# Performance work log

Hardware: AMD Instinct MI355X
Metric: run time of the kernel (lower is better)

The kernel has to match this reference:

```python
import jax, jax.numpy as jnp
import numpy as np

B, NV, DM, DK, DV, H, DFF = 256, 40, 512, 256, 256, 4, 2048
K1, K2 = 4, 8
EPS = 1e-5


def _knn_mask(vertices, k):
    # square_distance(xyz, xyz): dist[b,i,j] = ||x_i - x_j||^2
    d = -2.0 * jnp.einsum('bic,bjc->bij', vertices, vertices)
    sq = jnp.sum(vertices ** 2, -1)
    d = d + sq[:, :, None] + sq[:, None, :]
    # torch.topk(dist, k, dim=1, largest=False)[1].transpose(1,2) -> [B,N,k]
    idx = jax.lax.top_k(-jnp.swapaxes(d, 1, 2), k)[1]
    counts = jax.nn.one_hot(idx, NV, dtype=jnp.float32).sum(-2)  # [B,N,NV]
    return (counts < 1.0)[:, None, :, :]  # [B,1,N,N], broadcasts over heads (== repeat)


def _ln(x, g, b):
    m = x.mean(-1, keepdims=True)
    v = x.var(-1, keepdims=True)
    return (x - m) / jnp.sqrt(v + EPS) * g + b


def _encoder(x, mask, wq, bq, wk, bk, wv, bv, wo, bo, ln1g, ln1b, w1, b1, w2, b2, ln2g, ln2b):
    Bn, N, _ = x.shape
    q = (x @ wq + bq).reshape(Bn, N, H, DK).transpose(0, 2, 1, 3)   # [B,H,N,DK]
    kk = (x @ wk + bk).reshape(Bn, N, H, DK).transpose(0, 2, 3, 1)  # [B,H,DK,N]
    v = (x @ wv + bv).reshape(Bn, N, H, DV).transpose(0, 2, 1, 3)   # [B,H,N,DV]
    att = jnp.matmul(q, kk) / np.sqrt(DK)                           # [B,H,N,N]
    att = jnp.where(mask, -jnp.inf, att)
    att = jax.nn.softmax(att, axis=-1)
    o = jnp.matmul(att, v).transpose(0, 2, 1, 3).reshape(Bn, N, H * DV) @ wo + bo
    x = _ln(x + o, ln1g, ln1b)                                      # residual + LayerNorm
    ff = jax.nn.relu(x @ w1 + b1) @ w2 + b2                         # position-wise FFN
    return _ln(x + ff, ln2g, ln2b)


def _fusion(y, w1, b1, bng, bnb, w2, b2):
    y = y @ w1 + b1                       # Conv1d(1024,512,1) == per-position linear
    m = y.mean((0, 1))
    v = y.var((0, 1))                     # BatchNorm1d, training-mode batch stats (biased var)
    y = (y - m) / jnp.sqrt(v + EPS) * bng + bnb
    y = jnp.where(y > 0, y, 0.2 * y)      # LeakyReLU(0.2)
    return y @ w2 + b2                    # Conv1d(512,512,1)


def _forward(vertices, F, *p):
    m1 = _knn_mask(vertices, K1)
    m2 = _knn_mask(vertices, K2)
    F1 = _encoder(F, m1, *p[0:16])
    F2 = _encoder(F, m2, *p[16:32])
    yy = jnp.concatenate((F1, F2), -1)    # [B,N,2*DM]
    return _fusion(yy, *p[32:38])


def setup_inputs() -> dict:
    key = jax.random.key(0)
    d = {}
    cnt = [0]
    def nk():
        cnt[0] += 1
        return jax.random.fold_in(key, cnt[0])
    def lin(i, o):
        return jax.random.normal(nk(), (i, o), jnp.float32) * (1.0 / np.sqrt(i))
    d['vertices'] = jax.random.normal(nk(), (B, NV, 3), jnp.float32)
    d['F'] = jax.random.normal(nk(), (B, NV, DM), jnp.float32)
    for pfx in ('e1', 'e2'):
        d[pfx + '_wq'] = lin(DM, H * DK); d[pfx + '_bq'] = jnp.zeros((H * DK,), jnp.float32)
        d[pfx + '_wk'] = lin(DM, H * DK); d[pfx + '_bk'] = jnp.zeros((H * DK,), jnp.float32)
        d[pfx + '_wv'] = lin(DM, H * DV); d[pfx + '_bv'] = jnp.zeros((H * DV,), jnp.float32)
        d[pfx + '_wo'] = lin(H * DV, DM); d[pfx + '_bo'] = jnp.zeros((DM,), jnp.float32)
        d[pfx + '_ln1g'] = jnp.ones((DM,), jnp.float32); d[pfx + '_ln1b'] = jnp.zeros((DM,), jnp.float32)
        d[pfx + '_w1'] = lin(DM, DFF); d[pfx + '_b1'] = jnp.zeros((DFF,), jnp.float32)
        d[pfx + '_w2'] = lin(DFF, DM); d[pfx + '_b2'] = jnp.zeros((DM,), jnp.float32)
        d[pfx + '_ln2g'] = jnp.ones((DM,), jnp.float32); d[pfx + '_ln2b'] = jnp.zeros((DM,), jnp.float32)
    d['fus_w1'] = lin(2 * DM, DM); d['fus_b1'] = jnp.zeros((DM,), jnp.float32)
    d['fus_bng'] = jnp.ones((DM,), jnp.float32); d['fus_bnb'] = jnp.zeros((DM,), jnp.float32)
    d['fus_w2'] = lin(DM, DM); d['fus_b2'] = jnp.zeros((DM,), jnp.float32)
    return d


def reference(vertices, F,
              e1_wq, e1_bq, e1_wk, e1_bk, e1_wv, e1_bv, e1_wo, e1_bo,
              e1_ln1g, e1_ln1b, e1_w1, e1_b1, e1_w2, e1_b2, e1_ln2g, e1_ln2b,
              e2_wq, e2_bq, e2_wk, e2_bk, e2_wv, e2_bv, e2_wo, e2_bo,
              e2_ln1g, e2_ln1b, e2_w1, e2_b1, e2_w2, e2_b2, e2_ln2g, e2_ln2b,
              fus_w1, fus_b1, fus_bng, fus_bnb, fus_w2, fus_b2):
    return _forward(vertices, F,
                    e1_wq, e1_bq, e1_wk, e1_bk, e1_wv, e1_bv, e1_wo, e1_bo,
                    e1_ln1g, e1_ln1b, e1_w1, e1_b1, e1_w2, e1_b2, e1_ln2g, e1_ln2b,
                    e2_wq, e2_bq, e2_wk, e2_bk, e2_wv, e2_bv, e2_wo, e2_bo,
                    e2_ln1g, e2_ln1b, e2_w1, e2_b1, e2_w2, e2_b2, e2_ln2g, e2_ln2b,
                    fus_w1, fus_b1, fus_bng, fus_bnb, fus_w2, fus_b2)
```

## Files before the change

### kernel.cpp

```cpp
#include <hip/hip_runtime.h>

typedef unsigned short u16;
typedef unsigned int   u32;
typedef __attribute__((ext_vector_type(4))) float f32x4;
typedef __attribute__((ext_vector_type(8))) short short8;
typedef __attribute__((ext_vector_type(4))) unsigned short u16x4;

#define DEV __device__ __forceinline__
#define AS1 __attribute__((address_space(1)))
#define AS3 __attribute__((address_space(3)))

DEV float bf2f(u16 u){ return __uint_as_float(((u32)u)<<16); }
DEV u16 f2bf(float f){ u32 u=__float_as_uint(f); return (u16)((u + 0x7fffu + ((u>>16)&1u))>>16); }
DEV void g2lds16(const void* g, void* l){
  __builtin_amdgcn_global_load_lds((const AS1 void*)g, (AS3 void*)l, 16, 0, 0);
}

__global__ __launch_bounds__(256) void wt_kernel(const float* __restrict__ W,
                                                 u16* __restrict__ WT, int K, int N){
  __shared__ u16 tile[32][33];
  int n0 = blockIdx.x*32, k0 = blockIdx.y*32;
  int tx = threadIdx.x, ty = threadIdx.y;
  #pragma unroll
  for (int i=0;i<4;++i){
    int k = ty + i*8;
    tile[k][tx] = f2bf(W[(size_t)(k0+k)*N + n0 + tx]);
  }
  __syncthreads();
  #pragma unroll
  for (int i=0;i<4;++i){
    int n = ty + i*8;
    WT[(size_t)(n0+n)*K + k0 + tx] = tile[tx][n];
  }
}

__global__ __launch_bounds__(256) void cvt_kernel(const float* __restrict__ in,
                                                  u16* __restrict__ out, long n4){
  long i = ((long)blockIdx.x*256 + threadIdx.x);
  if (i < n4){
    f32x4 v = *(const f32x4*)(in + i*4);
    u16x4 r; r.x=f2bf(v.x); r.y=f2bf(v.y); r.z=f2bf(v.z); r.w=f2bf(v.w);
    *(u16x4*)(out + i*4) = r;
  }
}

__global__ __launch_bounds__(256) void catb_kernel(const float* __restrict__ a,
                                                   const float* __restrict__ b,
                                                   const float* __restrict__ c,
                                                   float* __restrict__ dst){
  int i = blockIdx.x*256 + threadIdx.x;
  if (i < 1024) dst[i] = a[i];
  else if (i < 2048) dst[i] = b[i-1024];
  else if (i < 3072) dst[i] = c[i-2048];
}

__global__ __launch_bounds__(256) void fill_kernel(float* p, float v, long n){
  long i = (long)blockIdx.x*256 + threadIdx.x;
  if (i < n) p[i] = v;
}

__global__ __launch_bounds__(256) void knn_kernel(const float* __restrict__ verts,
                                                  unsigned char* __restrict__ nbr1,
                                                  unsigned char* __restrict__ nbr2){
  __shared__ float P[40][3];
  __shared__ float SQ[40];
  int b = blockIdx.x, tid = threadIdx.x, wave = tid>>6, lane = tid&63;
  if (tid < 40){
    float x = verts[((size_t)b*40+tid)*3+0];
    float y = verts[((size_t)b*40+tid)*3+1];
    float z = verts[((size_t)b*40+tid)*3+2];
    P[tid][0]=x; P[tid][1]=y; P[tid][2]=z;
    SQ[tid] = __fadd_rn(__fadd_rn(__fmul_rn(x,x),__fmul_rn(y,y)),__fmul_rn(z,z));
  }
  __syncthreads();
  for (int i = wave; i < 40; i += 4){
    float d = 3.0e38f;
    if (lane < 40){
      int j = lane;
      float dot = __fadd_rn(__fadd_rn(__fmul_rn(P[i][0],P[j][0]),
                                      __fmul_rn(P[i][1],P[j][1])),
                            __fmul_rn(P[i][2],P[j][2]));
      d = __fadd_rn(__fadd_rn(__fmul_rn(-2.f,dot), SQ[j]), SQ[i]);
    }
    bool taken = false;
    #pragma unroll
    for (int s=0;s<8;++s){
      float v = taken ? 3.0e38f : d;
      float m = v;
      #pragma unroll
      for (int o=32;o;o>>=1) m = fminf(m, __shfl_xor(m, o));
      unsigned long long mask = __ballot(v == m);
      int bj = __ffsll((unsigned long long)mask) - 1;
      if (lane == bj) taken = true;
      if (lane == 0){
        if (s < 4) nbr1[((size_t)b*40+i)*4+s] = (unsigned char)bj;
        nbr2[((size_t)b*40+i)*8+s] = (unsigned char)bj;
      }
    }
  }
}

template<int RELU, int OUTBF>
__global__ __launch_bounds__(256, 4) void gemm_bt(const u16* __restrict__ A,
                                                  const u16* __restrict__ BT,
                                                  const float* __restrict__ bias,
                                                  void* __restrict__ Cout,
                                                  int M, int N, int K){
  __shared__ u16 As[128*32];
  __shared__ u16 Bs[128*32];
  const int tid  = threadIdx.x;
  const int wave = tid>>6, lane = tid&63;
  const int wr = (wave>>1)<<6, wc = (wave&1)<<6;
  const int row0 = blockIdx.x<<7, col0 = blockIdx.y<<7;
  f32x4 acc[4][4];
  #pragma unroll
  for (int i=0;i<4;++i)
    #pragma unroll
    for (int j=0;j<4;++j) acc[i][j] = (f32x4){0.f,0.f,0.f,0.f};

  const int rL = lane>>2;
  const int ch = lane&3;
  const int fr = lane&15, fc = lane>>4;
  const short8* Asv = (const short8*)As;
  const short8* Bsv = (const short8*)Bs;

  for (int kt=0; kt<K; kt+=32){
    #pragma unroll
    for (int c=0;c<2;++c){
      int lo = c*4096 + wave*1024;
      int r  = c*64 + wave*16 + rL;
      int kk = ((ch ^ ((r>>1)&3))<<3);
      g2lds16(A  + (size_t)(row0+r)*K + kt + kk, (char*)As + lo);
      g2lds16(BT + (size_t)(col0+r)*K + kt + kk, (char*)Bs + lo);
    }
    __syncthreads();
    short8 a[4], b[4];
    #pragma unroll
    for (int i=0;i<4;++i){
      int rowA = wr + i*16 + fr;
      int rowB = wc + i*16 + fr;
      a[i] = Asv[rowA*4 + (fc ^ ((rowA>>1)&3))];
      b[i] = Bsv[rowB*4 + (fc ^ ((rowB>>1)&3))];
    }
    #pragma unroll
    for (int i=0;i<4;++i)
      #pragma unroll
      for (int j=0;j<4;++j)
        acc[i][j] = __builtin_amdgcn_mfma_f32_16x16x32_bf16(a[i], b[j], acc[i][j], 0,0,0);
    __syncthreads();
  }
  #pragma unroll
  for (int i=0;i<4;++i){
    int mrow = row0 + wr + i*16 + fc*4;
    #pragma unroll
    for (int j=0;j<4;++j){
      int ncol = col0 + wc + j*16 + fr;
      float bv = bias[ncol];
      #pragma unroll
      for (int r=0;r<4;++r){
        float v = acc[i][j][r] + bv;
        if (RELU) v = v > 0.f ? v : 0.f;
        if (OUTBF) ((u16*)Cout)[(size_t)(mrow+r)*N + ncol] = f2bf(v);
        else       ((float*)Cout)[(size_t)(mrow+r)*N + ncol] = v;
      }
    }
  }
}

template<int KNB>
__global__ __launch_bounds__(256) void attn_kernel(const u16* __restrict__ QKV,
                                                   const unsigned char* __restrict__ nbr,
                                                   u16* __restrict__ O){
  __shared__ u16 KV[2][40*256];
  int b = blockIdx.x>>2, h = blockIdx.x&3;
  int tid = threadIdx.x, wave = tid>>6, lane = tid&63;
  const size_t rowb = (size_t)b*40;
  for (int c = tid; c < 1280; c += 256){
    int row = c >> 5, col = (c & 31) << 3;
    size_t src = (rowb+row)*3072 + h*256 + col;
    *(short8*)&KV[0][row*256+col] = *(const short8*)(QKV + src + 1024);
    *(short8*)&KV[1][row*256+col] = *(const short8*)(QKV + src + 2048);
  }
  __syncthreads();
  for (int i = wave; i < 40; i += 4){
    int js[KNB];
    if (KNB == 4){
      u32 p = *(const u32*)(nbr + (rowb+i)*4);
      js[0]=p&255; js[1]=(p>>8)&255; js[2]=(p>>16)&255; js[3]=(p>>24)&255;
    } else {
      u32 p0 = *(const u32*)(nbr + (rowb+i)*8);
      u32 p1 = *(const u32*)(nbr + (rowb+i)*8 + 4);
      js[0]=p0&255; js[1]=(p0>>8)&255; js[2]=(p0>>16)&255; js[3]=(p0>>24)&255;
      js[4]=p1&255; js[5]=(p1>>8)&255; js[6]=(p1>>16)&255; js[7]=(p1>>24)&255;
    }
    u16x4 qv = *(const u16x4*)(QKV + (rowb+i)*3072 + h*256 + lane*4);
    float q0=bf2f(qv.x), q1=bf2f(qv.y), q2=bf2f(qv.z), q3=bf2f(qv.w);
    float s[KNB];
    #pragma unroll
    for (int jj=0;jj<KNB;++jj){
      u16x4 kv = *(const u16x4*)&KV[0][js[jj]*256 + lane*4];
      s[jj] = q0*bf2f(kv.x) + q1*bf2f(kv.y) + q2*bf2f(kv.z) + q3*bf2f(kv.w);
    }
    #pragma unroll
    for (int jj=0;jj<KNB;++jj){
      #pragma unroll
      for (int o=32;o;o>>=1) s[jj] += __shfl_xor(s[jj], o);
      s[jj] *= 0.0625f;
    }
    float m = s[0];
    #pragma unroll
    for (int jj=1;jj<KNB;++jj) m = fmaxf(m, s[jj]);
    float sum = 0.f;
    #pragma unroll
    for (int jj=0;jj<KNB;++jj){ s[jj] = expf(s[jj]-m); sum += s[jj]; }
    float inv = 1.f/sum;
    float o0=0.f,o1=0.f,o2=0.f,o3=0.f;
    #pragma unroll
    for (int jj=0;jj<KNB;++jj){
      float w = s[jj]*inv;
      u16x4 vv = *(const u16x4*)&KV[1][js[jj]*256 + lane*4];
      o0 += w*bf2f(vv.x); o1 += w*bf2f(vv.y); o2 += w*bf2f(vv.z); o3 += w*bf2f(vv.w);
    }
    u16x4 r; r.x=f2bf(o0); r.y=f2bf(o1); r.z=f2bf(o2); r.w=f2bf(o3);
    *(u16x4*)(O + (rowb+i)*1024 + h*256 + lane*4) = r;
  }
}

DEV float blockReduce(float v, float* red){
  #pragma unroll
  for (int o=32;o;o>>=1) v += __shfl_xor(v, o);
  int lane = threadIdx.x&63, w = threadIdx.x>>6;
  if (lane==0) red[w] = v;
  __syncthreads();
  float t = red[0]+red[1]+red[2]+red[3];
  __syncthreads();
  return t;
}

__global__ __launch_bounds__(256) void ln_kernel(const float* __restrict__ resf,
                                                 const float* __restrict__ delta,
                                                 const float* __restrict__ g,
                                                 const float* __restrict__ be,
                                                 u16* __restrict__ outb, int ostride, int ocol,
                                                 float* __restrict__ outf){
  __shared__ float red[4];
  int row = blockIdx.x, tid = threadIdx.x;
  size_t ib = (size_t)row*512 + tid*2;
  float2 xr = *(const float2*)(resf+ib);
  float2 xd = *(const float2*)(delta+ib);
  float x0 = xr.x+xd.x, x1 = xr.y+xd.y;
  float s = blockReduce(x0+x1, red);
  float mean = s*(1.f/512.f);
  float d0 = x0-mean, d1 = x1-mean;
  float q = blockReduce(d0*d0+d1*d1, red);
  float inv = 1.f/sqrtf(q*(1.f/512.f)+1e-5f);
  float2 gg = *(const float2*)(g+tid*2);
  float2 bb = *(const float2*)(be+tid*2);
  float r0 = d0*inv*gg.x + bb.x;
  float r1 = d1*inv*gg.y + bb.y;
  size_t ob = (size_t)row*ostride + ocol + tid*2;
  *(u32*)(outb+ob) = ((u32)f2bf(r1)<<16) | (u32)f2bf(r0);
  if (outf){ *(float2*)(outf + ib) = make_float2(r0,r1); }
}

__global__ __launch_bounds__(512) void bn_part(const float* __restrict__ y,
                                               float* __restrict__ psum, float* __restrict__ psq){
  int c = threadIdx.x, blk = blockIdx.x;
  float s = 0.f, q = 0.f;
  for (int r = blk; r < 10240; r += 64){
    float v = y[(size_t)r*512 + c];
    s += v; q += v*v;
  }
  psum[blk*512+c] = s; psq[blk*512+c] = q;
}

__global__ __launch_bounds__(512) void bn_fin(const float* __restrict__ psum,
                                              const float* __restrict__ psq,
                                              const float* __restrict__ g,
                                              const float* __restrict__ b,
                                              float* __restrict__ scale, float* __restrict__ shift){
  int c = threadIdx.x;
  float s = 0.f, q = 0.f;
  for (int k=0;k<64;++k){ s += psum[k*512+c]; q += psq[k*512+c]; }
  float m = s*(1.f/10240.f);
  float var = q*(1.f/10240.f) - m*m;
  float sc = g[c]/sqrtf(var + 1e-5f);
  scale[c] = sc; shift[c] = b[c] - m*sc;
}

__global__ __launch_bounds__(256) void bn_apply(const float* __restrict__ y,
                                                const float* __restrict__ scale,
                                                const float* __restrict__ shift,
                                                u16* __restrict__ out){
  long i4 = ((long)blockIdx.x*256 + threadIdx.x)*4;
  if (i4 < (long)10240*512){
    int c = (int)(i4 & 511);
    f32x4 v  = *(const f32x4*)(y+i4);
    f32x4 sc = *(const f32x4*)(scale+c);
    f32x4 sh = *(const f32x4*)(shift+c);
    f32x4 r;
    #pragma unroll
    for (int k=0;k<4;++k){
      float t = v[k]*sc[k] + sh[k];
      r[k] = t > 0.f ? t : 0.2f*t;
    }
    u16x4 o; o.x=f2bf(r[0]); o.y=f2bf(r[1]); o.z=f2bf(r[2]); o.w=f2bf(r[3]);
    *(u16x4*)(out+i4) = o;
  }
}

extern "C" void kernel_launch(void* const* d_in, const int* in_sizes, int n_in,
                              void* d_out, int out_size, void* d_ws, size_t ws_size,
                              hipStream_t stream){
  const float* verts = (const float*)d_in[0];
  const float* F     = (const float*)d_in[1];
  const float* ew[2][16];
  for (int e=0;e<2;++e) for (int i=0;i<16;++i) ew[e][i] = (const float*)d_in[2+e*16+i];
  const float* fus_w1  = (const float*)d_in[34];
  const float* fus_b1  = (const float*)d_in[35];
  const float* fus_bng = (const float*)d_in[36];
  const float* fus_bnb = (const float*)d_in[37];
  const float* fus_w2  = (const float*)d_in[38];
  const float* fus_b2  = (const float*)d_in[39];

  const int M = 10240;
  size_t off = 0;
  auto alloc = [&](size_t bytes)->void*{
    void* p = (char*)d_ws + off; off = (off + bytes + 255) & ~(size_t)255; return p;
  };
  u16 *wtqkv[2],*wto[2],*wtw1[2],*wtw2[2];
  float* bqkv[2];
  for (int e=0;e<2;++e){
    wtqkv[e] = (u16*)alloc((size_t)3072*512*2);
    wto[e]   = (u16*)alloc((size_t)512*1024*2);
    wtw1[e]  = (u16*)alloc((size_t)2048*512*2);
    wtw2[e]  = (u16*)alloc((size_t)512*2048*2);
    bqkv[e]  = (float*)alloc(3072*4);
  }
  u16*  wtf1 = (u16*)alloc((size_t)512*1024*2);
  u16*  wtf2 = (u16*)alloc((size_t)512*512*2);
  u16*  Fb   = (u16*)alloc((size_t)M*512*2);
  u16*  QKVb = (u16*)alloc((size_t)M*3072*2);
  u16*  H1   = (u16*)alloc((size_t)M*2048*2);
  float* PF  = (float*)alloc((size_t)M*512*4);
  u16*  X1b  = (u16*)alloc((size_t)M*512*2);
  u16*  YC   = (u16*)alloc((size_t)M*1024*2);
  unsigned char* nbr1 = (unsigned char*)alloc(256*40*4);
  unsigned char* nbr2 = (unsigned char*)alloc(256*40*8);
  float* psum = (float*)alloc(64*512*4);
  float* psq  = (float*)alloc(64*512*4);
  float* bnsc = (float*)alloc(512*4);
  float* bnsh = (float*)alloc(512*4);
  u16*   OB  = H1;
  float* X1f = (float*)QKVb;
  float* Y1  = (float*)QKVb;
  u16*   Y2  = (u16*)((char*)QKVb + (size_t)M*512*4);

  if (off > ws_size){
    long n = out_size;
    fill_kernel<<<(unsigned)((n+255)/256),256,0,stream>>>((float*)d_out, 12345.0f, n);
    return;
  }

  for (int e=0;e<2;++e){
    wt_kernel<<<dim3(32,16),dim3(32,8),0,stream>>>(ew[e][0],  wtqkv[e],               512, 1024);
    wt_kernel<<<dim3(32,16),dim3(32,8),0,stream>>>(ew[e][2],  wtqkv[e]+(size_t)1024*512, 512, 1024);
    wt_kernel<<<dim3(32,16),dim3(32,8),0,stream>>>(ew[e][4],  wtqkv[e]+(size_t)2048*512, 512, 1024);
    wt_kernel<<<dim3(16,32),dim3(32,8),0,stream>>>(ew[e][6],  wto[e],  1024, 512);
    wt_kernel<<<dim3(64,16),dim3(32,8),0,stream>>>(ew[e][10], wtw1[e], 512, 2048);
    wt_kernel<<<dim3(16,64),dim3(32,8),0,stream>>>(ew[e][12], wtw2[e], 2048, 512);
    catb_kernel<<<12,256,0,stream>>>(ew[e][1], ew[e][3], ew[e][5], bqkv[e]);
  }
  wt_kernel<<<dim3(16,32),dim3(32,8),0,stream>>>(fus_w1, wtf1, 1024, 512);
  wt_kernel<<<dim3(16,16),dim3(32,8),0,stream>>>(fus_w2, wtf2, 512, 512);
  cvt_kernel<<<5120,256,0,stream>>>(F, Fb, (long)M*512/4);
  knn_kernel<<<256,256,0,stream>>>(verts, nbr1, nbr2);

  for (int e=0;e<2;++e){
    gemm_bt<0,1><<<dim3(80,24),256,0,stream>>>(Fb, wtqkv[e], bqkv[e], QKVb, M, 3072, 512);
    if (e == 0) attn_kernel<4><<<1024,256,0,stream>>>(QKVb, nbr1, OB);
    else        attn_kernel<8><<<1024,256,0,stream>>>(QKVb, nbr2, OB);
    gemm_bt<0,0><<<dim3(80,4),256,0,stream>>>(OB, wto[e], ew[e][7], PF, M, 512, 1024);
    ln_kernel<<<M,256,0,stream>>>(F, PF, ew[e][8], ew[e][9], X1b, 512, 0, X1f);
    gemm_bt<1,1><<<dim3(80,16),256,0,stream>>>(X1b, wtw1[e], ew[e][11], H1, M, 2048, 512);
    gemm_bt<0,0><<<dim3(80,4),256,0,stream>>>(H1, wtw2[e], ew[e][13], PF, M, 512, 2048);
    ln_kernel<<<M,256,0,stream>>>(X1f, PF, ew[e][14], ew[e][15], YC, 1024, e*512, nullptr);
  }

  gemm_bt<0,0><<<dim3(80,4),256,0,stream>>>(YC, wtf1, fus_b1, Y1, M, 512, 1024);
  bn_part<<<64,512,0,stream>>>(Y1, psum, psq);
  bn_fin<<<1,512,0,stream>>>(psum, psq, fus_bng, fus_bnb, bnsc, bnsh);
  bn_apply<<<5120,256,0,stream>>>(Y1, bnsc, bnsh, Y2);
  gemm_bt<0,0><<<dim3(80,4),256,0,stream>>>(Y2, wtf2, fus_b2, d_out, M, 512, 512);
}
```

Baseline: 560.0 us.

## Add 256x256-tile double-buffered GEMM for QKV and FFN1 projections

Adds a new bf16 MFMA GEMM kernel with 256x256 output tiles and 512 threads. It double-buffers 64-wide K slices into XOR-swizzled LDS using direct global-to-LDS loads, with explicit vmcnt waits and barriers so the next tile loads while the current one computes. The kernel replaces the 128-tile GEMM for the wide QKV (N=3072) and FFN-up (N=2048) projections, raising operand reuse per block. In exchange, the grid has fewer blocks (480 and 320), which risks under-filling the GPU's CUs, and register and LDS pressure are higher.

```diff
diff --git a/kernel.cpp b/kernel.cpp
--- a/kernel.cpp
+++ b/kernel.cpp
@@ -162,6 +162,110 @@
         if (RELU) v = v > 0.f ? v : 0.f;
         if (OUTBF) ((u16*)Cout)[(size_t)(mrow+r)*N + ncol] = f2bf(v);
         else       ((float*)Cout)[(size_t)(mrow+r)*N + ncol] = v;
+      }
+    }
+  }
+}
+
+DEV void stage_tile(const u16* __restrict__ G, int ldg, char* lds_buf,
+                    int row0, int k0, int w, int lane){
+  int cl = (lane&7) ^ (lane>>3);
+  const u16* src = G + (size_t)(row0 + w*8 + (lane>>3))*ldg + k0 + cl*8;
+  char* dst = lds_buf + w*1024;
+  #pragma unroll
+  for (int i=0;i<4;++i)
+    g2lds16(src + (size_t)i*64*ldg, dst + i*8192);
+}
+
+template<int RELU>
+__global__ __launch_bounds__(512, 2) void gemm256_bt(const u16* __restrict__ A,
+                                                     const u16* __restrict__ BT,
+                                                     const float* __restrict__ bias,
+                                                     u16* __restrict__ Cout,
+                                                     int M, int N, int K){
+  __shared__ u16 As[2][256*64];
+  __shared__ u16 Bs[2][256*64];
+  const int tid  = threadIdx.x;
+  const int wave = tid>>6, lane = tid&63;
+  const int wm = wave>>2, wn = wave&3;
+  const int fr = lane&15, fc = lane>>4;
+  const int row0 = blockIdx.x<<8, col0 = blockIdx.y<<8;
+  const int NT = K>>6;
+
+  f32x4 acc[8][4];
+  #pragma unroll
+  for (int i=0;i<8;++i)
+    #pragma unroll
+    for (int j=0;j<4;++j) acc[i][j] = (f32x4){0.f,0.f,0.f,0.f};
+
+  stage_tile(A,  K, (char*)As[0], row0, 0,  wave, lane);
+  stage_tile(BT, K, (char*)Bs[0], col0, 0,  wave, lane);
+  stage_tile(A,  K, (char*)As[1], row0, 64, wave, lane);
+  stage_tile(BT, K, (char*)Bs[1], col0, 64, wave, lane);
+
+  for (int t = 0; t < NT; ++t){
+    if (t+1 < NT) asm volatile("s_waitcnt vmcnt(8)" ::: "memory");
+    else          asm volatile("s_waitcnt vmcnt(0)" ::: "memory");
+    __builtin_amdgcn_sched_barrier(0);
+    __builtin_amdgcn_s_barrier();
+    __builtin_amdgcn_sched_barrier(0);
+
+    const short8* AV = (const short8*)As[t&1];
+    const short8* BV = (const short8*)Bs[t&1];
+    short8 b[4][2];
+    #pragma unroll
+    for (int nf=0;nf<4;++nf){
+      int rr = wn*64 + nf*16 + fr;
+      #pragma unroll
+      for (int kk=0;kk<2;++kk){
+        int cl = kk*4 + fc;
+        b[nf][kk] = BV[rr*8 + (cl ^ (rr&7))];
+      }
+    }
+    #pragma unroll
+    for (int q=0;q<4;++q){
+      short8 a[2][2];
+      #pragma unroll
+      for (int m2=0;m2<2;++m2){
+        int rr = wm*128 + (q*2+m2)*16 + fr;
+        #pragma unroll
+        for (int kk=0;kk<2;++kk){
+          int cl = kk*4 + fc;
+          a[m2][kk] = AV[rr*8 + (cl ^ (rr&7))];
+        }
+      }
+      __builtin_amdgcn_s_setprio(1);
+      #pragma unroll
+      for (int m2=0;m2<2;++m2)
+        #pragma unroll
+        for (int nf=0;nf<4;++nf){
+          acc[q*2+m2][nf] = __builtin_amdgcn_mfma_f32_16x16x32_bf16(a[m2][0], b[nf][0], acc[q*2+m2][nf], 0,0,0);
+          acc[q*2+m2][nf] = __builtin_amdgcn_mfma_f32_16x16x32_bf16(a[m2][1], b[nf][1], acc[q*2+m2][nf], 0,0,0);
+        }
+      __builtin_amdgcn_s_setprio(0);
+    }
+
+    __builtin_amdgcn_sched_barrier(0);
+    __builtin_amdgcn_s_barrier();
+    __builtin_amdgcn_sched_barrier(0);
+    if (t+2 < NT){
+      stage_tile(A,  K, (char*)As[t&1], row0, (t+2)<<6, wave, lane);
+      stage_tile(BT, K, (char*)Bs[t&1], col0, (t+2)<<6, wave, lane);
+    }
+  }
+
+  #pragma unroll
+  for (int i=0;i<8;++i){
+    int mrow = row0 + wm*128 + i*16 + fc*4;
+    #pragma unroll
+    for (int j=0;j<4;++j){
+      int ncol = col0 + wn*64 + j*16 + fr;
+      float bv = bias[ncol];
+      #pragma unroll
+      for (int r=0;r<4;++r){
+        float v = acc[i][j][r] + bv;
+        if (RELU) v = v > 0.f ? v : 0.f;
+        Cout[(size_t)(mrow+r)*N + ncol] = f2bf(v);
       }
     }
   }
@@ -377,12 +481,12 @@
   knn_kernel<<<256,256,0,stream>>>(verts, nbr1, nbr2);
 
   for (int e=0;e<2;++e){
-    gemm_bt<0,1><<<dim3(80,24),256,0,stream>>>(Fb, wtqkv[e], bqkv[e], QKVb, M, 3072, 512);
+    gemm256_bt<0><<<dim3(40,12),512,0,stream>>>(Fb, wtqkv[e], bqkv[e], QKVb, M, 3072, 512);
     if (e == 0) attn_kernel<4><<<1024,256,0,stream>>>(QKVb, nbr1, OB);
     else        attn_kernel<8><<<1024,256,0,stream>>>(QKVb, nbr2, OB);
     gemm_bt<0,0><<<dim3(80,4),256,0,stream>>>(OB, wto[e], ew[e][7], PF, M, 512, 1024);
     ln_kernel<<<M,256,0,stream>>>(F, PF, ew[e][8], ew[e][9], X1b, 512, 0, X1f);
-    gemm_bt<1,1><<<dim3(80,16),256,0,stream>>>(X1b, wtw1[e], ew[e][11], H1, M, 2048, 512);
+    gemm256_bt<1><<<dim3(40,8),512,0,stream>>>(X1b, wtw1[e], ew[e][11], H1, M, 2048, 512);
     gemm_bt<0,0><<<dim3(80,4),256,0,stream>>>(H1, wtw2[e], ew[e][13], PF, M, 512, 2048);
     ln_kernel<<<M,256,0,stream>>>(X1f, PF, ew[e][14], ew[e][15], YC, 1024, e*512, nullptr);
   }
```

Result: slower. 571.8 us (+2.1%).

## Add 256x256 four-stage pipelined GEMM for QKV and FFN1, batch weight transposes

Applied to the files above, without the earlier changes.

Adds a new 512-thread GEMM kernel with 256x256 output tiles, a 4-deep LDS ring fed by direct global-to-LDS loads, XOR-swizzled LDS layout, explicit vmcnt waits and setprio around MFMA blocks. The kernel is used for the wide QKV and FFN-up projections to raise data reuse per tile and hide load latency. Separately, the 14 weight-transpose launches are merged into one launch driven by a job table to cut launch overhead. With one workgroup per CU and large tiles, the grids shrink to 480 and 320 blocks, so the gain depends on full CU occupancy and correct pipeline synchronisation.

```diff
diff --git a/kernel.cpp b/kernel.cpp
--- a/kernel.cpp
+++ b/kernel.cpp
@@ -9,6 +9,8 @@
 #define DEV __device__ __forceinline__
 #define AS1 __attribute__((address_space(1)))
 #define AS3 __attribute__((address_space(3)))
+#define SB  __builtin_amdgcn_sched_barrier(0)
+#define BAR __builtin_amdgcn_s_barrier()
 
 DEV float bf2f(u16 u){ return __uint_as_float(((u32)u)<<16); }
 DEV u16 f2bf(float f){ u32 u=__float_as_uint(f); return (u16)((u + 0x7fffu + ((u>>16)&1u))>>16); }
@@ -16,10 +18,26 @@
   __builtin_amdgcn_global_load_lds((const AS1 void*)g, (AS3 void*)l, 16, 0, 0);
 }
 
-__global__ __launch_bounds__(256) void wt_kernel(const float* __restrict__ W,
-                                                 u16* __restrict__ WT, int K, int N){
+struct WtJobs {
+  const float* W[14];
+  u16*         WT[14];
+  int K[14];
+  int N[14];
+  int off[15];
+};
+
+__global__ __launch_bounds__(256) void wtb_kernel(WtJobs J){
   __shared__ u16 tile[32][33];
-  int n0 = blockIdx.x*32, k0 = blockIdx.y*32;
+  int bid = blockIdx.x;
+  int j = 0;
+  #pragma unroll
+  for (int s=1;s<14;++s) if (bid >= J.off[s]) j = s;
+  int lb = bid - J.off[j];
+  int K = J.K[j], N = J.N[j];
+  int nx = N>>5;
+  int n0 = (lb % nx)<<5, k0 = (lb / nx)<<5;
+  const float* W = J.W[j];
+  u16* WT = J.WT[j];
   int tx = threadIdx.x, ty = threadIdx.y;
   #pragma unroll
   for (int i=0;i<4;++i){
@@ -162,6 +180,101 @@
         if (RELU) v = v > 0.f ? v : 0.f;
         if (OUTBF) ((u16*)Cout)[(size_t)(mrow+r)*N + ncol] = f2bf(v);
         else       ((float*)Cout)[(size_t)(mrow+r)*N + ncol] = v;
+      }
+    }
+  }
+}
+
+DEV void stage32(const u16* __restrict__ gbase, int ldg, u16* __restrict__ buf,
+                 int kt, int wave, int lane){
+  int srw = wave*16 + (lane>>2);
+  int scl = (lane&3) ^ ((srw>>1)&3);
+  const u16* src = gbase + (size_t)srw*ldg + kt + scl*8;
+  char* dst = (char*)buf + wave*1024;
+  g2lds16(src, dst);
+  g2lds16(src + (size_t)128*ldg, dst + 8192);
+}
+
+template<int RELU>
+__global__ __launch_bounds__(512, 1) void gemm256p(const u16* __restrict__ A,
+                                                   const u16* __restrict__ BT,
+                                                   const float* __restrict__ bias,
+                                                   u16* __restrict__ Cout,
+                                                   int M, int N, int K){
+  __shared__ u16 As[4][256*32];
+  __shared__ u16 Bs[4][256*32];
+  const int tid  = threadIdx.x;
+  const int wave = tid>>6, lane = tid&63;
+  const int wm = wave>>2, wn = wave&3;
+  const int fr = lane&15, fc = lane>>4;
+  const int row0 = blockIdx.x<<8, col0 = blockIdx.y<<8;
+  const int NT = K>>5;
+  const u16* Ag = A  + (size_t)row0*K;
+  const u16* Bg = BT + (size_t)col0*K;
+
+  f32x4 acc[8][4];
+  #pragma unroll
+  for (int i=0;i<8;++i)
+    #pragma unroll
+    for (int j=0;j<4;++j) acc[i][j] = (f32x4){0.f,0.f,0.f,0.f};
+
+  stage32(Ag, K, As[0], 0,  wave, lane);  stage32(Bg, K, Bs[0], 0,  wave, lane);
+  stage32(Ag, K, As[1], 32, wave, lane);  stage32(Bg, K, Bs[1], 32, wave, lane);
+  stage32(Ag, K, As[2], 64, wave, lane);  stage32(Bg, K, Bs[2], 64, wave, lane);
+  asm volatile("s_waitcnt vmcnt(8)" ::: "memory");
+  SB; BAR; SB;
+
+  for (int t = 0; t < NT; ++t){
+    const int cur = t&3, nx3 = (t+3)&3;
+    const short8* AV = (const short8*)As[cur];
+    const short8* BV = (const short8*)Bs[cur];
+    short8 a[4], b[4];
+    #pragma unroll
+    for (int nf=0;nf<4;++nf){ int rr = wn*64 + nf*16 + fr; b[nf] = BV[rr*4 + (fc ^ ((rr>>1)&3))]; }
+    #pragma unroll
+    for (int mf=0;mf<4;++mf){ int rr = wm*128 + mf*16 + fr; a[mf] = AV[rr*4 + (fc ^ ((rr>>1)&3))]; }
+    if (t+3 < NT) stage32(Ag, K, As[nx3], (t+3)<<5, wave, lane);
+    SB; BAR; SB;
+    __builtin_amdgcn_s_setprio(1);
+    #pragma unroll
+    for (int mf=0;mf<4;++mf)
+      #pragma unroll
+      for (int nf=0;nf<4;++nf)
+        acc[mf][nf] = __builtin_amdgcn_mfma_f32_16x16x32_bf16(a[mf], b[nf], acc[mf][nf], 0,0,0);
+    __builtin_amdgcn_s_setprio(0);
+    SB; BAR; SB;
+    #pragma unroll
+    for (int mf=0;mf<4;++mf){ int rr = wm*128 + (mf+4)*16 + fr; a[mf] = AV[rr*4 + (fc ^ ((rr>>1)&3))]; }
+    if (t+3 < NT) stage32(Bg, K, Bs[nx3], (t+3)<<5, wave, lane);
+    {
+      int rem = NT - t - 1;
+      if (rem >= 3)      asm volatile("s_waitcnt vmcnt(8)" ::: "memory");
+      else if (rem == 2) asm volatile("s_waitcnt vmcnt(4)" ::: "memory");
+      else if (rem == 1) asm volatile("s_waitcnt vmcnt(0)" ::: "memory");
+    }
+    SB; BAR; SB;
+    __builtin_amdgcn_s_setprio(1);
+    #pragma unroll
+    for (int mf=0;mf<4;++mf)
+      #pragma unroll
+      for (int nf=0;nf<4;++nf)
+        acc[mf+4][nf] = __builtin_amdgcn_mfma_f32_16x16x32_bf16(a[mf], b[nf], acc[mf+4][nf], 0,0,0);
+    __builtin_amdgcn_s_setprio(0);
+    SB; BAR; SB;
+  }
+
+  #pragma unroll
+  for (int i=0;i<8;++i){
+    int mrow = row0 + wm*128 + i*16 + fc*4;
+    #pragma unroll
+    for (int j=0;j<4;++j){
+      int ncol = col0 + wn*64 + j*16 + fr;
+      float bv = bias[ncol];
+      #pragma unroll
+      for (int r=0;r<4;++r){
+        float v = acc[i][j][r] + bv;
+        if (RELU) v = v > 0.f ? v : 0.f;
+        Cout[(size_t)(mrow+r)*N + ncol] = f2bf(v);
       }
     }
   }
@@ -362,27 +475,36 @@
     return;
   }
 
+  WtJobs J;
+  int nb = 0, ji = 0;
+  auto addjob = [&](const float* W, u16* WT, int K, int N){
+    J.W[ji]=W; J.WT[ji]=WT; J.K[ji]=K; J.N[ji]=N; J.off[ji]=nb;
+    nb += (N>>5)*(K>>5); ++ji;
+  };
   for (int e=0;e<2;++e){
-    wt_kernel<<<dim3(32,16),dim3(32,8),0,stream>>>(ew[e][0],  wtqkv[e],               512, 1024);
-    wt_kernel<<<dim3(32,16),dim3(32,8),0,stream>>>(ew[e][2],  wtqkv[e]+(size_t)1024*512, 512, 1024);
-    wt_kernel<<<dim3(32,16),dim3(32,8),0,stream>>>(ew[e][4],  wtqkv[e]+(size_t)2048*512, 512, 1024);
-    wt_kernel<<<dim3(16,32),dim3(32,8),0,stream>>>(ew[e][6],  wto[e],  1024, 512);
-    wt_kernel<<<dim3(64,16),dim3(32,8),0,stream>>>(ew[e][10], wtw1[e], 512, 2048);
-    wt_kernel<<<dim3(16,64),dim3(32,8),0,stream>>>(ew[e][12], wtw2[e], 2048, 512);
+    addjob(ew[e][0],  wtqkv[e],                    512, 1024);
+    addjob(ew[e][2],  wtqkv[e]+(size_t)1024*512,   512, 1024);
+    addjob(ew[e][4],  wtqkv[e]+(size_t)2048*512,   512, 1024);
+    addjob(ew[e][6],  wto[e],  1024, 512);
+    addjob(ew[e][10], wtw1[e], 512, 2048);
+    addjob(ew[e][12], wtw2[e], 2048, 512);
+  }
+  addjob(fus_w1, wtf1, 1024, 512);
+  addjob(fus_w2, wtf2, 512, 512);
+  J.off[14] = nb;
+  wtb_kernel<<<nb, dim3(32,8), 0, stream>>>(J);
+  for (int e=0;e<2;++e)
     catb_kernel<<<12,256,0,stream>>>(ew[e][1], ew[e][3], ew[e][5], bqkv[e]);
-  }
-  wt_kernel<<<dim3(16,32),dim3(32,8),0,stream>>>(fus_w1, wtf1, 1024, 512);
-  wt_kernel<<<dim3(16,16),dim3(32,8),0,stream>>>(fus_w2, wtf2, 512, 512);
   cvt_kernel<<<5120,256,0,stream>>>(F, Fb, (long)M*512/4);
   knn_kernel<<<256,256,0,stream>>>(verts, nbr1, nbr2);
 
   for (int e=0;e<2;++e){
-    gemm_bt<0,1><<<dim3(80,24),256,0,stream>>>(Fb, wtqkv[e], bqkv[e], QKVb, M, 3072, 512);
+    gemm256p<0><<<dim3(40,12),512,0,stream>>>(Fb, wtqkv[e], bqkv[e], QKVb, M, 3072, 512);
     if (e == 0) attn_kernel<4><<<1024,256,0,stream>>>(QKVb, nbr1, OB);
     else        attn_kernel<8><<<1024,256,0,stream>>>(QKVb, nbr2, OB);
     gemm_bt<0,0><<<dim3(80,4),256,0,stream>>>(OB, wto[e], ew[e][7], PF, M, 512, 1024);
     ln_kernel<<<M,256,0,stream>>>(F, PF, ew[e][8], ew[e][9], X1b, 512, 0, X1f);
-    gemm_bt<1,1><<<dim3(80,16),256,0,stream>>>(X1b, wtw1[e], ew[e][11], H1, M, 2048, 512);
+    gemm256p<1><<<dim3(40,8),512,0,stream>>>(X1b, wtw1[e], ew[e][11], H1, M, 2048, 512);
     gemm_bt<0,0><<<dim3(80,4),256,0,stream>>>(H1, wtw2[e], ew[e][13], PF, M, 512, 2048);
     ln_kernel<<<M,256,0,stream>>>(X1f, PF, ew[e][14], ew[e][15], YC, 1024, e*512, nullptr);
   }
```

Result: no change. 551.9 us (-1.4%).
